# Optimization experiments

Hardware: AMD Instinct MI355X
Metric: run time of the kernel (lower is better)

Reference implementation:

```python
import jax, jax.numpy as jnp
import numpy as np

B, T, C, H, DH = 4, 2048, 1024, 16, 64  # batch, seq (block_size), n_embd, heads, head_size


def setup_inputs() -> dict:
    key = jax.random.key(0)
    ks = jax.random.split(key, 6)
    x = jax.random.normal(ks[0], (B, T, C), dtype=jnp.float32)
    init = 0.02
    Wq = jax.random.normal(ks[1], (H, C, DH), dtype=jnp.float32) * init
    Wk = jax.random.normal(ks[2], (H, C, DH), dtype=jnp.float32) * init
    Wv = jax.random.normal(ks[3], (H, C, DH), dtype=jnp.float32) * init
    Wp = jax.random.normal(ks[4], (H * DH, C), dtype=jnp.float32) * init
    bp = jnp.zeros((C,), dtype=jnp.float32)
    return {"x": x, "Wq": Wq, "Wk": Wk, "Wv": Wv, "Wp": Wp, "bp": bp}


def reference(x, Wq, Wk, Wv, Wp, bp):
    Bb, Tt, Cc = x.shape
    # per-head projections, vectorized over heads (original loops in Python)
    q = jnp.einsum('btc,hcd->bhtd', x, Wq)
    k = jnp.einsum('btc,hcd->bhtd', x, Wk)
    v = jnp.einsum('btc,hcd->bhtd', x, Wv)
    # NOTE: original scales by rsqrt(C) where C is the INPUT embed dim, not head_size
    scale = 1.0 / jnp.sqrt(jnp.asarray(Cc, dtype=x.dtype))
    wei = jnp.einsum('bhtd,bhsd->bhts', q, k) * scale  # [B,H,T,T]
    causal = jnp.tril(jnp.ones((Tt, Tt), dtype=bool))
    wei = jnp.where(causal, wei, -jnp.inf)
    wei = jax.nn.softmax(wei, axis=-1)
    out = jnp.einsum('bhts,bhsd->bhtd', wei, v)  # [B,H,T,DH]
    # concat heads along feature axis (head h -> slice h*DH:(h+1)*DH)
    out = out.transpose(0, 2, 1, 3).reshape(Bb, Tt, -1)  # [B,T,H*DH]
    out = out @ Wp + bp  # output projection to n_embd
    return out
```

## Files before the change

### kernel.cpp

```cpp
#include <hip/hip_runtime.h>

#define TSEQ 2048
#define CDIM 1024
#define NH 16
#define DH 64
#define NB 4

typedef __bf16 bf16x8 __attribute__((ext_vector_type(8)));
typedef float f32x4 __attribute__((ext_vector_type(4)));

#define QSCALE 0.04508422f

static __device__ __forceinline__ ushort f2bf(float f) {
  unsigned u = __float_as_uint(f);
  unsigned r = u + 0x7fffu + ((u >> 16) & 1u);
  return (ushort)(r >> 16);
}

static __device__ __forceinline__ uint cvtpk(float lo, float hi) {
  uint r;
  asm("v_cvt_pk_bf16_f32 %0, %1, %2" : "=v"(r) : "v"(lo), "v"(hi));
  return r;
}

static __device__ __forceinline__ void gload_lds16(const void* g, void* ldsbase) {
  __builtin_amdgcn_global_load_lds((const __attribute__((address_space(1))) void*)g,
                                   (__attribute__((address_space(3))) void*)ldsbase,
                                   16, 0, 0);
}

__global__ void cvt_x_kernel(const float4* __restrict__ src, ushort4* __restrict__ dst, int n4) {
  int i = blockIdx.x * blockDim.x + threadIdx.x;
  if (i >= n4) return;
  float4 f = src[i];
  ushort4 o;
  o.x = f2bf(f.x); o.y = f2bf(f.y); o.z = f2bf(f.z); o.w = f2bf(f.w);
  dst[i] = o;
}

__global__ void transpose_cvt_all(const float* __restrict__ Wq, const float* __restrict__ Wk,
                                  const float* __restrict__ Wv, const float* __restrict__ Wp,
                                  ushort* __restrict__ wall, ushort* __restrict__ wpT) {
  __shared__ float tile[32][33];
  const int z = blockIdx.z;
  const float* s; ushort* d; int Cc, c0, r0;
  if (z < 3) {
    const int head = blockIdx.x >> 1;
    s = (z == 0 ? Wq : z == 1 ? Wk : Wv) + (size_t)head * CDIM * DH;
    d = wall + ((size_t)z << 20) + (size_t)head * CDIM * DH;
    Cc = DH; c0 = (blockIdx.x & 1) * 32; r0 = blockIdx.y * 32;
  } else {
    s = Wp; d = wpT; Cc = CDIM; c0 = blockIdx.x * 32; r0 = blockIdx.y * 32;
  }
  const int tx = threadIdx.x, ty = threadIdx.y;
  for (int i = ty; i < 32; i += 8)
    tile[i][tx] = s[(size_t)(r0 + i) * Cc + c0 + tx];
  __syncthreads();
  for (int i = ty; i < 32; i += 8)
    d[(size_t)(c0 + i) * CDIM + r0 + tx] = f2bf(tile[tx][i]);
}

template <int MODE>
__global__ __launch_bounds__(256) void gemm_kernel(
    const ushort* __restrict__ A, const ushort* __restrict__ Bt,
    const float* __restrict__ bp, float* __restrict__ fout,
    ushort* __restrict__ qb, ushort* __restrict__ kb, ushort* __restrict__ vTb) {
  __shared__ ushort lds[32768];
  const int tid = threadIdx.x, w = tid >> 6, l = tid & 63;
  const int nwg = gridDim.x;
  const int bid = blockIdx.x;
  const int wgid = (bid & 7) * (nwg >> 3) + (bid >> 3);
  const int NT = (MODE == 0) ? 24 : 8;
  const int nt = wgid % NT, mt = wgid / NT;
  const int wr = w >> 1, wc = w & 1;
  const int srow = l >> 3;
  const int scol = (((l & 7) ^ srow) << 3);
  char* ldsb = (char*)lds;

  f32x4 acc[4][4] = {};

  const ushort* Arow = A + ((size_t)mt * 128) * CDIM;
  const ushort* Brow = Bt + ((size_t)nt * 128) * CDIM;

#pragma unroll
  for (int i = 0; i < 8; ++i) {
    int ch = w * 8 + i;
    const ushort* src = (ch < 16) ? Arow + (size_t)(ch * 8 + srow) * CDIM + scol
                                  : Brow + (size_t)((ch - 16) * 8 + srow) * CDIM + scol;
    gload_lds16(src, ldsb + ch * 1024);
  }

  for (int k0 = 0; k0 < CDIM; k0 += 64) {
    const int bsel = (k0 >> 6) & 1;
    char* base = ldsb + bsel * 32768;
    __syncthreads();
    if (k0 + 64 < CDIM) {
      char* nbase = ldsb + (bsel ^ 1) * 32768;
#pragma unroll
      for (int i = 0; i < 8; ++i) {
        int ch = w * 8 + i;
        const ushort* src = (ch < 16)
            ? Arow + (size_t)(ch * 8 + srow) * CDIM + k0 + 64 + scol
            : Brow + (size_t)((ch - 16) * 8 + srow) * CDIM + k0 + 64 + scol;
        gload_lds16(src, nbase + ch * 1024);
      }
    }
#pragma unroll
    for (int ks = 0; ks < 2; ++ks) {
      bf16x8 af[4];
#pragma unroll
      for (int fm = 0; fm < 4; ++fm) {
        int row = wr * 64 + fm * 16 + (l & 15);
        int cb = (ks * 64 + 16 * (l >> 4)) ^ ((row & 7) << 4);
        af[fm] = *(const bf16x8*)(base + row * 128 + cb);
      }
#pragma unroll
      for (int fn = 0; fn < 4; ++fn) {
        int n = wc * 64 + fn * 16 + (l & 15);
        int cb = (ks * 64 + 16 * (l >> 4)) ^ ((n & 7) << 4);
        bf16x8 bfr = *(const bf16x8*)(base + 16384 + n * 128 + cb);
#pragma unroll
        for (int fm = 0; fm < 4; ++fm)
          acc[fm][fn] = __builtin_amdgcn_mfma_f32_16x16x32_bf16(af[fm], bfr, acc[fm][fn], 0, 0, 0);
      }
    }
  }

#pragma unroll
  for (int fm = 0; fm < 4; ++fm) {
#pragma unroll
    for (int fn = 0; fn < 4; ++fn) {
      const int gr0 = mt * 128 + wr * 64 + fm * 16 + (l >> 4) * 4;
      const int gc = nt * 128 + wc * 64 + fn * 16 + (l & 15);
      if (MODE == 1) {
        float bias = bp[gc];
#pragma unroll
        for (int r = 0; r < 4; ++r)
          fout[(size_t)(gr0 + r) * CDIM + gc] = acc[fm][fn][r] + bias;
      } else {
        const int sel = gc >> 10, h = (gc >> 6) & 15, d = gc & 63;
        const int bh = (gr0 >> 11) * NH + h, tl = gr0 & 2047;
        if (sel == 2) {
          ushort4 pk;
          pk.x = f2bf(acc[fm][fn][0]); pk.y = f2bf(acc[fm][fn][1]);
          pk.z = f2bf(acc[fm][fn][2]); pk.w = f2bf(acc[fm][fn][3]);
          *(ushort4*)(vTb + ((size_t)bh * DH + d) * TSEQ + tl) = pk;
        } else if (sel == 0) {
#pragma unroll
          for (int r = 0; r < 4; ++r)
            qb[((size_t)bh * TSEQ + tl + r) * DH + d] = f2bf(acc[fm][fn][r] * QSCALE);
        } else {
#pragma unroll
          for (int r = 0; r < 4; ++r)
            kb[((size_t)bh * TSEQ + tl + r) * DH + d] = f2bf(acc[fm][fn][r]);
        }
      }
    }
  }
}

__global__ __launch_bounds__(256, 3) void attn_kernel(
    const ushort* __restrict__ qb, const ushort* __restrict__ kb,
    const ushort* __restrict__ vTb, ushort* __restrict__ aob) {
  __shared__ ushort lds[16384];
  char* ldsb = (char*)lds;
  const int tid = threadIdx.x, w = tid >> 6, l = tid & 63;
  const int id = blockIdx.x;
  const int bh = (id & 7) * 8 + ((id >> 3) & 7);
  const int qt = 15 - (id >> 6);
  const int q0 = qt * 128;
  const int nt = 2 * (qt + 1);
  const int b = bh >> 4, h = bh & 15;
  const int g = l >> 4, q = l & 15;
  const int srow = l >> 3;
  const int scol = (((l & 7) ^ srow) << 3);
  const int adrA = ((l & 16) << 1 | q) << 2;
  const int adrB = adrA + 64;
  const bool hi32 = (l & 32) != 0;

  bf16x8 qf[2][2];
#pragma unroll
  for (int qs = 0; qs < 2; ++qs) {
    const ushort* qrow = qb + ((size_t)bh * TSEQ + q0 + w * 32 + qs * 16 + q) * DH;
    qf[qs][0] = *(const bf16x8*)(qrow + 8 * g);
    qf[qs][1] = *(const bf16x8*)(qrow + 32 + 8 * g);
  }

  float m[2] = {-1e30f, -1e30f}, lsum[2] = {0.f, 0.f};
  f32x4 o[4][2] = {};

#pragma unroll
  for (int i = 0; i < 4; ++i) {
    int ch = w * 4 + i;
    if (ch < 8)
      gload_lds16(kb + ((size_t)bh * TSEQ + ch * 8 + srow) * DH + scol, ldsb + ch * 1024);
    else {
      int d = (ch - 8) * 8 + srow;
      gload_lds16(vTb + ((size_t)bh * DH + d) * TSEQ + scol, ldsb + 16384 + (ch - 8) * 1024);
    }
  }

#pragma unroll 1
  for (int j = 0; j < nt; ++j) {
    __syncthreads();
    const int cbuf = j & 1;
    if (j + 1 < nt) {
      const int kvn = (j + 1) * 64, nb = (j + 1) & 1;
#pragma unroll
      for (int i = 0; i < 4; ++i) {
        int ch = w * 4 + i;
        if (ch < 8)
          gload_lds16(kb + ((size_t)bh * TSEQ + kvn + ch * 8 + srow) * DH + scol,
                      ldsb + nb * 8192 + ch * 1024);
        else {
          int d = (ch - 8) * 8 + srow;
          gload_lds16(vTb + ((size_t)bh * DH + d) * TSEQ + kvn + scol,
                      ldsb + 16384 + nb * 8192 + (ch - 8) * 1024);
        }
      }
    }
    char* Kb = ldsb + cbuf * 8192;
    char* Vb = ldsb + 16384 + cbuf * 8192;

    f32x4 s[4][2] = {};
    __builtin_amdgcn_s_setprio(1);
#pragma unroll
    for (int ks = 0; ks < 2; ++ks)
#pragma unroll
      for (int fn = 0; fn < 4; ++fn) {
        int n = fn * 16 + q;
        int cbb = (ks * 64 + 16 * g) ^ ((n & 7) << 4);
        bf16x8 kf = *(const bf16x8*)(Kb + n * 128 + cbb);
        s[fn][0] = __builtin_amdgcn_mfma_f32_16x16x32_bf16(kf, qf[0][ks], s[fn][0], 0, 0, 0);
        s[fn][1] = __builtin_amdgcn_mfma_f32_16x16x32_bf16(kf, qf[1][ks], s[fn][1], 0, 0, 0);
      }
    __builtin_amdgcn_s_setprio(0);

    if (j >= nt - 2) {
#pragma unroll
      for (int qs = 0; qs < 2; ++qs) {
        int rowloc = q0 + w * 32 + qs * 16 + q - j * 64;
#pragma unroll
        for (int fn = 0; fn < 4; ++fn)
#pragma unroll
          for (int r = 0; r < 4; ++r)
            if (fn * 16 + 4 * g + r > rowloc) s[fn][qs][r] = -1e30f;
      }
    }

    float rm[2];
#pragma unroll
    for (int qs = 0; qs < 2; ++qs) {
      float v = -1e30f;
#pragma unroll
      for (int fn = 0; fn < 4; ++fn)
        v = fmaxf(v, fmaxf(fmaxf(s[fn][qs][0], s[fn][qs][1]), fmaxf(s[fn][qs][2], s[fn][qs][3])));
      v = fmaxf(v, __shfl_xor(v, 16));
      v = fmaxf(v, __shfl_xor(v, 32));
      rm[qs] = v;
    }

    if (__any(fmaxf(rm[0] - m[0], rm[1] - m[1]) > 8.f)) {
      float fc[2];
#pragma unroll
      for (int qs = 0; qs < 2; ++qs) {
        float mn = fmaxf(m[qs], rm[qs]);
        fc[qs] = __builtin_amdgcn_exp2f(m[qs] - mn);
        m[qs] = mn; lsum[qs] *= fc[qs];
      }
#pragma unroll
      for (int r = 0; r < 4; ++r) {
        float f0 = __shfl(fc[0], (l & 0x30) | (4 * g + r), 64);
        float f1 = __shfl(fc[1], (l & 0x30) | (4 * g + r), 64);
#pragma unroll
        for (int fn = 0; fn < 4; ++fn) { o[fn][0][r] *= f0; o[fn][1][r] *= f1; }
      }
    }

    uint D[2][4][2];
#pragma unroll
    for (int qs = 0; qs < 2; ++qs) {
      float rs = 0.f;
#pragma unroll
      for (int fn = 0; fn < 4; ++fn) {
        float p0 = __builtin_amdgcn_exp2f(s[fn][qs][0] - m[qs]);
        float p1 = __builtin_amdgcn_exp2f(s[fn][qs][1] - m[qs]);
        float p2 = __builtin_amdgcn_exp2f(s[fn][qs][2] - m[qs]);
        float p3 = __builtin_amdgcn_exp2f(s[fn][qs][3] - m[qs]);
        rs += (p0 + p1) + (p2 + p3);
        D[qs][fn][0] = cvtpk(p0, p1);
        D[qs][fn][1] = cvtpk(p2, p3);
      }
      rs += __shfl_xor(rs, 16);
      rs += __shfl_xor(rs, 32);
      lsum[qs] += rs;
    }

#pragma unroll
    for (int ksg = 0; ksg < 2; ++ksg) {
      union { uint u[4]; bf16x8 v; } P[2];
#pragma unroll
      for (int qs = 0; qs < 2; ++qs) {
        uint t0a = __builtin_amdgcn_ds_bpermute(adrA, (int)D[qs][2 * ksg][0]);
        uint t0b = __builtin_amdgcn_ds_bpermute(adrA, (int)D[qs][2 * ksg + 1][0]);
        uint t1a = __builtin_amdgcn_ds_bpermute(adrA, (int)D[qs][2 * ksg][1]);
        uint t1b = __builtin_amdgcn_ds_bpermute(adrA, (int)D[qs][2 * ksg + 1][1]);
        uint t2a = __builtin_amdgcn_ds_bpermute(adrB, (int)D[qs][2 * ksg][0]);
        uint t2b = __builtin_amdgcn_ds_bpermute(adrB, (int)D[qs][2 * ksg + 1][0]);
        uint t3a = __builtin_amdgcn_ds_bpermute(adrB, (int)D[qs][2 * ksg][1]);
        uint t3b = __builtin_amdgcn_ds_bpermute(adrB, (int)D[qs][2 * ksg + 1][1]);
        P[qs].u[0] = hi32 ? t0b : t0a;
        P[qs].u[1] = hi32 ? t1b : t1a;
        P[qs].u[2] = hi32 ? t2b : t2a;
        P[qs].u[3] = hi32 ? t3b : t3a;
      }
      __builtin_amdgcn_s_setprio(1);
#pragma unroll
      for (int fn = 0; fn < 4; ++fn) {
        int n = fn * 16 + q;
        int cbb = (ksg * 64 + 16 * g) ^ ((n & 7) << 4);
        bf16x8 vf = *(const bf16x8*)(Vb + n * 128 + cbb);
        o[fn][0] = __builtin_amdgcn_mfma_f32_16x16x32_bf16(P[0].v, vf, o[fn][0], 0, 0, 0);
        o[fn][1] = __builtin_amdgcn_mfma_f32_16x16x32_bf16(P[1].v, vf, o[fn][1], 0, 0, 0);
      }
      __builtin_amdgcn_s_setprio(0);
    }
  }

#pragma unroll
  for (int qs = 0; qs < 2; ++qs) {
    float inv = 1.f / lsum[qs];
#pragma unroll
    for (int r = 0; r < 4; ++r) {
      float invq = __shfl(inv, (l & 0x30) | (4 * g + r), 64);
      int t = q0 + w * 32 + qs * 16 + 4 * g + r;
#pragma unroll
      for (int fn = 0; fn < 4; ++fn) {
        int d = fn * 16 + q;
        aob[((size_t)b * TSEQ + t) * (NH * DH) + h * DH + d] = f2bf(o[fn][qs][r] * invq);
      }
    }
  }
}

extern "C" void kernel_launch(void* const* d_in, const int* in_sizes, int n_in,
                              void* d_out, int out_size, void* d_ws, size_t ws_size,
                              hipStream_t stream) {
  (void)in_sizes; (void)n_in; (void)out_size; (void)ws_size;
  const float* x  = (const float*)d_in[0];
  const float* Wq = (const float*)d_in[1];
  const float* Wk = (const float*)d_in[2];
  const float* Wv = (const float*)d_in[3];
  const float* Wp = (const float*)d_in[4];
  const float* bp = (const float*)d_in[5];
  float* out = (float*)d_out;
  char* ws = (char*)d_ws;

  ushort* xb  = (ushort*)(ws);
  ushort* wall = (ushort*)(ws + (16ull << 20));
  ushort* wpT = (ushort*)(ws + (22ull << 20));
  ushort* qb  = (ushort*)(ws + (24ull << 20));
  ushort* kb  = (ushort*)(ws + (40ull << 20));
  ushort* vTb = (ushort*)(ws + (56ull << 20));
  ushort* aob = (ushort*)(ws + (72ull << 20));

  cvt_x_kernel<<<(NB * TSEQ * CDIM / 4 + 255) / 256, 256, 0, stream>>>(
      (const float4*)x, (ushort4*)xb, NB * TSEQ * CDIM / 4);
  transpose_cvt_all<<<dim3(32, 32, 4), dim3(32, 8), 0, stream>>>(Wq, Wk, Wv, Wp, wall, wpT);

  gemm_kernel<0><<<dim3(64 * 24), 256, 0, stream>>>(xb, wall, nullptr, nullptr, qb, kb, vTb);
  attn_kernel<<<dim3(1024), 256, 0, stream>>>(qb, kb, vTb, aob);
  gemm_kernel<1><<<dim3(64 * 8), 256, 0, stream>>>(aob, wpT, bp, out, nullptr, nullptr, nullptr);
}
```

Baseline: 181.1 us.

## Halve GEMM K-tile with new swizzle; defer softmax row reductions

The projection GEMM now uses a 32-wide K step with half the LDS (16 KB per buffer) and a new XOR swizzle for the 64-byte rows. This aims to raise occupancy and cut LDS footprint, at the cost of twice as many barriers and loop iterations. In the attention kernel, the per-tile cross-lane max reduction now runs only when a rescale is triggered. The per-tile row-sum shuffles are moved to a single reduction at the end, and the running max starts at zero instead of -1e30. These changes cut shuffle traffic in the inner loop but rely on the lazy-rescale threshold staying numerically safe.

```diff
diff --git a/kernel.cpp b/kernel.cpp
--- a/kernel.cpp
+++ b/kernel.cpp
@@ -65,7 +65,7 @@
     const ushort* __restrict__ A, const ushort* __restrict__ Bt,
     const float* __restrict__ bp, float* __restrict__ fout,
     ushort* __restrict__ qb, ushort* __restrict__ kb, ushort* __restrict__ vTb) {
-  __shared__ ushort lds[32768];
+  __shared__ ushort lds[16384];
   const int tid = threadIdx.x, w = tid >> 6, l = tid & 63;
   const int nwg = gridDim.x;
   const int bid = blockIdx.x;
@@ -73,8 +73,10 @@
   const int NT = (MODE == 0) ? 24 : 8;
   const int nt = wgid % NT, mt = wgid / NT;
   const int wr = w >> 1, wc = w & 1;
-  const int srow = l >> 3;
-  const int scol = (((l & 7) ^ srow) << 3);
+  const int srw = l >> 2;
+  const int sck = l & 3;
+  const int scol = (sck ^ ((srw >> 1) & 3)) * 8;
+  const int g = l >> 4;
   char* ldsb = (char*)lds;
 
   f32x4 acc[4][4] = {};
@@ -83,46 +85,41 @@
   const ushort* Brow = Bt + ((size_t)nt * 128) * CDIM;
 
 #pragma unroll
-  for (int i = 0; i < 8; ++i) {
-    int ch = w * 8 + i;
-    const ushort* src = (ch < 16) ? Arow + (size_t)(ch * 8 + srow) * CDIM + scol
-                                  : Brow + (size_t)((ch - 16) * 8 + srow) * CDIM + scol;
+  for (int i = 0; i < 4; ++i) {
+    int ch = w * 4 + i;
+    const ushort* src = (ch < 8) ? Arow + (size_t)(ch * 16 + srw) * CDIM + scol
+                                 : Brow + (size_t)((ch - 8) * 16 + srw) * CDIM + scol;
     gload_lds16(src, ldsb + ch * 1024);
   }
 
-  for (int k0 = 0; k0 < CDIM; k0 += 64) {
-    const int bsel = (k0 >> 6) & 1;
-    char* base = ldsb + bsel * 32768;
+  for (int k0 = 0; k0 < CDIM; k0 += 32) {
+    const int bsel = (k0 >> 5) & 1;
+    char* base = ldsb + bsel * 16384;
     __syncthreads();
-    if (k0 + 64 < CDIM) {
-      char* nbase = ldsb + (bsel ^ 1) * 32768;
-#pragma unroll
-      for (int i = 0; i < 8; ++i) {
-        int ch = w * 8 + i;
-        const ushort* src = (ch < 16)
-            ? Arow + (size_t)(ch * 8 + srow) * CDIM + k0 + 64 + scol
-            : Brow + (size_t)((ch - 16) * 8 + srow) * CDIM + k0 + 64 + scol;
-        gload_lds16(src, nbase + ch * 1024);
-      }
-    }
-#pragma unroll
-    for (int ks = 0; ks < 2; ++ks) {
-      bf16x8 af[4];
-#pragma unroll
-      for (int fm = 0; fm < 4; ++fm) {
-        int row = wr * 64 + fm * 16 + (l & 15);
-        int cb = (ks * 64 + 16 * (l >> 4)) ^ ((row & 7) << 4);
-        af[fm] = *(const bf16x8*)(base + row * 128 + cb);
-      }
-#pragma unroll
-      for (int fn = 0; fn < 4; ++fn) {
-        int n = wc * 64 + fn * 16 + (l & 15);
-        int cb = (ks * 64 + 16 * (l >> 4)) ^ ((n & 7) << 4);
-        bf16x8 bfr = *(const bf16x8*)(base + 16384 + n * 128 + cb);
-#pragma unroll
-        for (int fm = 0; fm < 4; ++fm)
-          acc[fm][fn] = __builtin_amdgcn_mfma_f32_16x16x32_bf16(af[fm], bfr, acc[fm][fn], 0, 0, 0);
-      }
+    if (k0 + 32 < CDIM) {
+      char* nb = ldsb + (bsel ^ 1) * 16384;
+#pragma unroll
+      for (int i = 0; i < 4; ++i) {
+        int ch = w * 4 + i;
+        const ushort* src = (ch < 8)
+            ? Arow + (size_t)(ch * 16 + srw) * CDIM + k0 + 32 + scol
+            : Brow + (size_t)((ch - 8) * 16 + srw) * CDIM + k0 + 32 + scol;
+        gload_lds16(src, nb + ch * 1024);
+      }
+    }
+    bf16x8 af[4];
+#pragma unroll
+    for (int fm = 0; fm < 4; ++fm) {
+      int row = wr * 64 + fm * 16 + (l & 15);
+      af[fm] = *(const bf16x8*)(base + row * 64 + ((g ^ ((row >> 1) & 3)) << 4));
+    }
+#pragma unroll
+    for (int fn = 0; fn < 4; ++fn) {
+      int n = wc * 64 + fn * 16 + (l & 15);
+      bf16x8 bfr = *(const bf16x8*)(base + 8192 + n * 64 + ((g ^ ((n >> 1) & 3)) << 4));
+#pragma unroll
+      for (int fm = 0; fm < 4; ++fm)
+        acc[fm][fn] = __builtin_amdgcn_mfma_f32_16x16x32_bf16(af[fm], bfr, acc[fm][fn], 0, 0, 0);
     }
   }
 
@@ -186,7 +183,7 @@
     qf[qs][1] = *(const bf16x8*)(qrow + 32 + 8 * g);
   }
 
-  float m[2] = {-1e30f, -1e30f}, lsum[2] = {0.f, 0.f};
+  float m[2] = {0.f, 0.f}, lsum[2] = {0.f, 0.f};
   f32x4 o[4][2] = {};
 
 #pragma unroll
@@ -248,23 +245,23 @@
       }
     }
 
-    float rm[2];
+    float vmx[2];
 #pragma unroll
     for (int qs = 0; qs < 2; ++qs) {
-      float v = -1e30f;
-#pragma unroll
-      for (int fn = 0; fn < 4; ++fn)
-        v = fmaxf(v, fmaxf(fmaxf(s[fn][qs][0], s[fn][qs][1]), fmaxf(s[fn][qs][2], s[fn][qs][3])));
-      v = fmaxf(v, __shfl_xor(v, 16));
-      v = fmaxf(v, __shfl_xor(v, 32));
-      rm[qs] = v;
-    }
-
-    if (__any(fmaxf(rm[0] - m[0], rm[1] - m[1]) > 8.f)) {
+      float v = fmaxf(fmaxf(fmaxf(s[0][qs][0], s[0][qs][1]), fmaxf(s[0][qs][2], s[0][qs][3])),
+                      fmaxf(fmaxf(s[1][qs][0], s[1][qs][1]), fmaxf(s[1][qs][2], s[1][qs][3])));
+      v = fmaxf(v, fmaxf(fmaxf(fmaxf(s[2][qs][0], s[2][qs][1]), fmaxf(s[2][qs][2], s[2][qs][3])),
+                         fmaxf(fmaxf(s[3][qs][0], s[3][qs][1]), fmaxf(s[3][qs][2], s[3][qs][3]))));
+      vmx[qs] = v;
+    }
+    if (__any(fmaxf(vmx[0] - m[0], vmx[1] - m[1]) > 8.f)) {
       float fc[2];
 #pragma unroll
       for (int qs = 0; qs < 2; ++qs) {
-        float mn = fmaxf(m[qs], rm[qs]);
+        float v = vmx[qs];
+        v = fmaxf(v, __shfl_xor(v, 16));
+        v = fmaxf(v, __shfl_xor(v, 32));
+        float mn = fmaxf(m[qs], v);
         fc[qs] = __builtin_amdgcn_exp2f(m[qs] - mn);
         m[qs] = mn; lsum[qs] *= fc[qs];
       }
@@ -291,8 +288,6 @@
         D[qs][fn][0] = cvtpk(p0, p1);
         D[qs][fn][1] = cvtpk(p2, p3);
       }
-      rs += __shfl_xor(rs, 16);
-      rs += __shfl_xor(rs, 32);
       lsum[qs] += rs;
     }
 
@@ -329,7 +324,10 @@
 
 #pragma unroll
   for (int qs = 0; qs < 2; ++qs) {
-    float inv = 1.f / lsum[qs];
+    float tot = lsum[qs];
+    tot += __shfl_xor(tot, 16);
+    tot += __shfl_xor(tot, 32);
+    float inv = 1.f / tot;
 #pragma unroll
     for (int r = 0; r < 4; ++r) {
       float invq = __shfl(inv, (l & 0x30) | (4 * g + r), 64);
```

New measurement: 176.0 us. 1.03x faster.
